# Kernel optimization log

Measured on AMD Instinct MI355X. Metric: run time of the kernel, lower is better.

## Reference

```python
import jax, jax.numpy as jnp
import numpy as np

N_NODES = 100000
N_EDGES = 800000
D_COORD = 16
N_FEAT = 8
D_IN = D_COORD * 2 + N_FEAT  # 40
H = 64
D_OUT = 16


def _mlp_params(key, sizes):
    ps = []
    for i, (a, b) in enumerate(zip(sizes[:-1], sizes[1:])):
        key, k = jax.random.split(key)
        # lecun_normal: std = 1/sqrt(fan_in)
        W = jax.random.normal(k, (a, b), dtype=jnp.float32) / jnp.sqrt(jnp.float32(a))
        ps.append(W)
        ps.append(jnp.zeros((b,), dtype=jnp.float32))
    return key, ps


def setup_inputs() -> dict:
    key = jax.random.key(0)
    k1, k2, k3, k4, key = jax.random.split(key, 5)
    coordinates = jax.random.normal(k1, (N_NODES, D_COORD), dtype=jnp.float32)
    feature_array = jax.random.normal(k2, (N_EDGES, N_FEAT), dtype=jnp.float32)
    non_fictitious = jnp.ones((N_EDGES,), dtype=jnp.float32)
    addr_from = jax.random.randint(k3, (N_EDGES,), 0, N_NODES, dtype=jnp.int32)
    addr_to = jax.random.randint(k4, (N_EDGES,), 0, N_NODES, dtype=jnp.int32)
    sizes = [D_IN, H, H, D_OUT]
    key, pf = _mlp_params(key, sizes)
    key, pt = _mlp_params(key, sizes)
    fW0, fb0, fW1, fb1, fW2, fb2 = pf
    tW0, tb0, tW1, tb1, tW2, tb2 = pt
    return dict(coordinates=coordinates, feature_array=feature_array,
                non_fictitious=non_fictitious, addr_from=addr_from, addr_to=addr_to,
                fW0=fW0, fb0=fb0, fW1=fW1, fb1=fb1, fW2=fW2, fb2=fb2,
                tW0=tW0, tb0=tb0, tW1=tW1, tb1=tb1, tW2=tW2, tb2=tb2)


def _mlp(x, W0, b0, W1, b1, W2, b2):
    # hidden activations = relu, final_activation = None
    h = jax.nn.relu(x @ W0 + b0)
    h = jax.nn.relu(h @ W1 + b1)
    return h @ W2 + b2


def reference(coordinates, feature_array, non_fictitious, addr_from, addr_to,
              fW0, fb0, fW1, fb1, fW2, fb2, tW0, tb0, tW1, tb1, tW2, tb2):
    # Shared edge input: [E, N_FEAT + 2*D_COORD] = concat(features, x_from, x_to)
    inp = jnp.concatenate(
        [feature_array, coordinates[addr_from], coordinates[addr_to]], axis=-1)
    mask = non_fictitious[:, None]  # [E, 1]
    inp = inp * mask
    acc = jnp.zeros((coordinates.shape[0], D_OUT), dtype=coordinates.dtype)
    # port 'from': its own MLP, scatter-add to addr_from
    out_f = _mlp(inp, fW0, fb0, fW1, fb1, fW2, fb2) * mask
    acc = acc.at[addr_from].add(out_f)
    # port 'to': its own MLP, scatter-add to addr_to
    out_t = _mlp(inp, tW0, tb0, tW1, tb1, tW2, tb2) * mask
    acc = acc.at[addr_to].add(out_t)
    # outer_activation = tanh
    return jnp.tanh(acc)
```

## Files before the change

### kernel.cpp

```cpp
#include <hip/hip_runtime.h>
#include <math.h>

constexpr int N_EDGES = 800000;
constexpr int D_COORD = 16;
constexpr int N_FEAT  = 8;
constexpr int D_IN    = 40;
constexpr int H       = 64;
constexpr int D_OUT   = 16;
constexpr int ET      = 64;
constexpr int XP      = 68;

__global__ __launch_bounds__(256) void edge_mlp_tiled(
    const float* __restrict__ coords,
    const float* __restrict__ feat,
    const float* __restrict__ mask,
    const int*   __restrict__ a_from,
    const int*   __restrict__ a_to,
    const float* __restrict__ fW0, const float* __restrict__ fb0,
    const float* __restrict__ fW1, const float* __restrict__ fb1,
    const float* __restrict__ fW2, const float* __restrict__ fb2,
    const float* __restrict__ tW0, const float* __restrict__ tb0,
    const float* __restrict__ tW1, const float* __restrict__ tb1,
    const float* __restrict__ tW2, const float* __restrict__ tb2,
    float* __restrict__ acc_out)
{
    __shared__ float Xs[D_IN * XP];
    __shared__ float Ws[H * H];
    __shared__ float Hs[H * XP];
    __shared__ float ms[ET];
    __shared__ int   nodes[2][ET];

    const int tid = threadIdx.x;
    const int e0  = blockIdx.x * ET;

    if (tid < ET) {
        ms[tid]       = mask[e0 + tid];
        nodes[0][tid] = a_from[e0 + tid];
        nodes[1][tid] = a_to[e0 + tid];
    }
    if (tid < 128) {
        const int e = tid >> 1, half = tid & 1;
        const float m = mask[e0 + e];
        float4 v = reinterpret_cast<const float4*>(feat)[(size_t)(e0 + e) * 2 + half];
        const int r = half * 4;
        Xs[(r + 0) * XP + e] = v.x * m;
        Xs[(r + 1) * XP + e] = v.y * m;
        Xs[(r + 2) * XP + e] = v.z * m;
        Xs[(r + 3) * XP + e] = v.w * m;
    }
    {
        const int e = tid >> 2, q = tid & 3;
        const float m = mask[e0 + e];
        const int nf = a_from[e0 + e];
        const int nt = a_to[e0 + e];
        float4 cf = reinterpret_cast<const float4*>(coords)[(size_t)nf * 4 + q];
        float4 ct = reinterpret_cast<const float4*>(coords)[(size_t)nt * 4 + q];
        const int rf = 8 + q * 4, rt = 24 + q * 4;
        Xs[(rf + 0) * XP + e] = cf.x * m;
        Xs[(rf + 1) * XP + e] = cf.y * m;
        Xs[(rf + 2) * XP + e] = cf.z * m;
        Xs[(rf + 3) * XP + e] = cf.w * m;
        Xs[(rt + 0) * XP + e] = ct.x * m;
        Xs[(rt + 1) * XP + e] = ct.y * m;
        Xs[(rt + 2) * XP + e] = ct.z * m;
        Xs[(rt + 3) * XP + e] = ct.w * m;
    }

    const int tx = tid & 15, ty = tid >> 4;

    auto run_mlp = [&](const float* __restrict__ W0, const float* __restrict__ b0,
                       const float* __restrict__ W1, const float* __restrict__ b1,
                       const float* __restrict__ W2, const float* __restrict__ b2,
                       const int which)
    {
        float a[4][4];

        __syncthreads();
        {
            const float4* s4 = reinterpret_cast<const float4*>(W0);
            float4* d4 = reinterpret_cast<float4*>(Ws);
            #pragma unroll
            for (int i = 0; i < (D_IN * H / 4 + 255) / 256; ++i) {
                int idx = tid + i * 256;
                if (idx < D_IN * H / 4) d4[idx] = s4[idx];
            }
        }
        __syncthreads();

        {
            float4 bv = reinterpret_cast<const float4*>(b0)[tx];
            #pragma unroll
            for (int i = 0; i < 4; ++i) {
                a[i][0] = bv.x; a[i][1] = bv.y; a[i][2] = bv.z; a[i][3] = bv.w;
            }
            #pragma unroll 8
            for (int k = 0; k < D_IN; ++k) {
                float4 xv = *reinterpret_cast<const float4*>(&Xs[k * XP + ty * 4]);
                float4 wv = *reinterpret_cast<const float4*>(&Ws[k * H + tx * 4]);
                const float xc[4] = {xv.x, xv.y, xv.z, xv.w};
                const float wc[4] = {wv.x, wv.y, wv.z, wv.w};
                #pragma unroll
                for (int i = 0; i < 4; ++i)
                    #pragma unroll
                    for (int j = 0; j < 4; ++j)
                        a[i][j] = fmaf(xc[i], wc[j], a[i][j]);
            }
            #pragma unroll
            for (int i = 0; i < 4; ++i)
                #pragma unroll
                for (int j = 0; j < 4; ++j)
                    a[i][j] = fmaxf(a[i][j], 0.0f);
        }
        __syncthreads();

        #pragma unroll
        for (int j = 0; j < 4; ++j) {
            const int r = tx * 4 + j;
            float4 hv = make_float4(a[0][j], a[1][j], a[2][j], a[3][j]);
            *reinterpret_cast<float4*>(&Hs[r * XP + ty * 4]) = hv;
        }
        {
            const float4* s4 = reinterpret_cast<const float4*>(W1);
            float4* d4 = reinterpret_cast<float4*>(Ws);
            #pragma unroll
            for (int i = 0; i < H * H / 4 / 256; ++i)
                d4[tid + i * 256] = s4[tid + i * 256];
        }
        __syncthreads();

        {
            float4 bv = reinterpret_cast<const float4*>(b1)[tx];
            float acc2[4][4];
            #pragma unroll
            for (int i = 0; i < 4; ++i) {
                acc2[i][0] = bv.x; acc2[i][1] = bv.y; acc2[i][2] = bv.z; acc2[i][3] = bv.w;
            }
            #pragma unroll 8
            for (int k = 0; k < H; ++k) {
                float4 xv = *reinterpret_cast<const float4*>(&Hs[k * XP + ty * 4]);
                float4 wv = *reinterpret_cast<const float4*>(&Ws[k * H + tx * 4]);
                const float xc[4] = {xv.x, xv.y, xv.z, xv.w};
                const float wc[4] = {wv.x, wv.y, wv.z, wv.w};
                #pragma unroll
                for (int i = 0; i < 4; ++i)
                    #pragma unroll
                    for (int j = 0; j < 4; ++j)
                        acc2[i][j] = fmaf(xc[i], wc[j], acc2[i][j]);
            }
            #pragma unroll
            for (int i = 0; i < 4; ++i)
                #pragma unroll
                for (int j = 0; j < 4; ++j)
                    a[i][j] = fmaxf(acc2[i][j], 0.0f);
        }
        __syncthreads();

        #pragma unroll
        for (int j = 0; j < 4; ++j) {
            const int r = tx * 4 + j;
            float4 hv = make_float4(a[0][j], a[1][j], a[2][j], a[3][j]);
            *reinterpret_cast<float4*>(&Hs[r * XP + ty * 4]) = hv;
        }
        {
            const float4* s4 = reinterpret_cast<const float4*>(W2);
            float4* d4 = reinterpret_cast<float4*>(Ws);
            if (tid < H * D_OUT / 4) d4[tid] = s4[tid];
        }
        __syncthreads();

        {
            const int ox = tid & 15, ey = tid >> 4;
            float o[4];
            const float bo = b2[ox];
            #pragma unroll
            for (int i = 0; i < 4; ++i) o[i] = bo;
            #pragma unroll 8
            for (int k = 0; k < H; ++k) {
                float4 xv = *reinterpret_cast<const float4*>(&Hs[k * XP + ey * 4]);
                const float wv = Ws[k * D_OUT + ox];
                o[0] = fmaf(xv.x, wv, o[0]);
                o[1] = fmaf(xv.y, wv, o[1]);
                o[2] = fmaf(xv.z, wv, o[2]);
                o[3] = fmaf(xv.w, wv, o[3]);
            }
            #pragma unroll
            for (int i = 0; i < 4; ++i) {
                const int e = ey * 4 + i;
                const float m = ms[e];
                const int node = nodes[which][e];
                atomicAdd(acc_out + (size_t)node * D_OUT + ox, o[i] * m);
            }
        }
    };

    run_mlp(fW0, fb0, fW1, fb1, fW2, fb2, 0);
    run_mlp(tW0, tb0, tW1, tb1, tW2, tb2, 1);
}

__global__ __launch_bounds__(256) void tanh_inplace(float* __restrict__ p, int n4)
{
    const int i = blockIdx.x * blockDim.x + threadIdx.x;
    if (i >= n4) return;
    float4 v = reinterpret_cast<float4*>(p)[i];
    v.x = tanhf(v.x); v.y = tanhf(v.y); v.z = tanhf(v.z); v.w = tanhf(v.w);
    reinterpret_cast<float4*>(p)[i] = v;
}

extern "C" void kernel_launch(void* const* d_in, const int* in_sizes, int n_in,
                              void* d_out, int out_size, void* d_ws, size_t ws_size,
                              hipStream_t stream)
{
    const float* coords = (const float*)d_in[0];
    const float* feat   = (const float*)d_in[1];
    const float* mask   = (const float*)d_in[2];
    const int*   a_from = (const int*)d_in[3];
    const int*   a_to   = (const int*)d_in[4];
    const float* fW0 = (const float*)d_in[5];
    const float* fb0 = (const float*)d_in[6];
    const float* fW1 = (const float*)d_in[7];
    const float* fb1 = (const float*)d_in[8];
    const float* fW2 = (const float*)d_in[9];
    const float* fb2 = (const float*)d_in[10];
    const float* tW0 = (const float*)d_in[11];
    const float* tb0 = (const float*)d_in[12];
    const float* tW1 = (const float*)d_in[13];
    const float* tb1 = (const float*)d_in[14];
    const float* tW2 = (const float*)d_in[15];
    const float* tb2 = (const float*)d_in[16];

    float* out = (float*)d_out;

    hipMemsetAsync(out, 0, (size_t)out_size * sizeof(float), stream);

    edge_mlp_tiled<<<N_EDGES / ET, 256, 0, stream>>>(
        coords, feat, mask, a_from, a_to,
        fW0, fb0, fW1, fb1, fW2, fb2,
        tW0, tb0, tW1, tb1, tW2, tb2, out);

    const int n4 = out_size / 4;
    tanh_inplace<<<(n4 + 255) / 256, 256, 0, stream>>>(out, n4);
}
```

Baseline: 472.9 us.

## Read MLP weights as wave-uniform scalar loads and double edges per block

Stops staging weights in shared memory. Each wavefront now owns a 16-column output slice, and its weights are read straight from global memory with wave-uniform indices, so they can become scalar loads. The edge tile grows from 64 to 128 edges per block, each lane computes 2 edges, and a launch-bounds occupancy hint is added. This removes the weight-copy stages and their barriers, at the cost of more accumulator registers per lane and reliance on the scalar cache holding the weights.

```diff
diff --git a/kernel.cpp b/kernel.cpp
--- a/kernel.cpp
+++ b/kernel.cpp
@@ -2,15 +2,12 @@
 #include <math.h>
 
 constexpr int N_EDGES = 800000;
-constexpr int D_COORD = 16;
-constexpr int N_FEAT  = 8;
 constexpr int D_IN    = 40;
 constexpr int H       = 64;
 constexpr int D_OUT   = 16;
-constexpr int ET      = 64;
-constexpr int XP      = 68;
-
-__global__ __launch_bounds__(256) void edge_mlp_tiled(
+constexpr int EB      = 128;
+
+__global__ __launch_bounds__(256, 2) void edge_mlp_v3(
     const float* __restrict__ coords,
     const float* __restrict__ feat,
     const float* __restrict__ mask,
@@ -24,171 +21,136 @@
     const float* __restrict__ tW2, const float* __restrict__ tb2,
     float* __restrict__ acc_out)
 {
-    __shared__ float Xs[D_IN * XP];
-    __shared__ float Ws[H * H];
-    __shared__ float Hs[H * XP];
-    __shared__ float ms[ET];
-    __shared__ int   nodes[2][ET];
-
-    const int tid = threadIdx.x;
-    const int e0  = blockIdx.x * ET;
-
-    if (tid < ET) {
+    __shared__ float Xs[D_IN * EB];
+    __shared__ float Hs[H * EB];
+    __shared__ float ms[EB];
+    __shared__ int   nodes[2][EB];
+
+    const int tid  = threadIdx.x;
+    const int lane = tid & 63;
+    const int uwid = __builtin_amdgcn_readfirstlane(tid >> 6);
+    const int e0   = blockIdx.x * EB;
+
+    if (tid < EB) {
         ms[tid]       = mask[e0 + tid];
         nodes[0][tid] = a_from[e0 + tid];
         nodes[1][tid] = a_to[e0 + tid];
     }
-    if (tid < 128) {
+    {
         const int e = tid >> 1, half = tid & 1;
         const float m = mask[e0 + e];
         float4 v = reinterpret_cast<const float4*>(feat)[(size_t)(e0 + e) * 2 + half];
         const int r = half * 4;
-        Xs[(r + 0) * XP + e] = v.x * m;
-        Xs[(r + 1) * XP + e] = v.y * m;
-        Xs[(r + 2) * XP + e] = v.z * m;
-        Xs[(r + 3) * XP + e] = v.w * m;
+        Xs[(r + 0) * EB + e] = v.x * m;
+        Xs[(r + 1) * EB + e] = v.y * m;
+        Xs[(r + 2) * EB + e] = v.z * m;
+        Xs[(r + 3) * EB + e] = v.w * m;
     }
     {
-        const int e = tid >> 2, q = tid & 3;
+        const int e = tid >> 1, which = tid & 1;
         const float m = mask[e0 + e];
-        const int nf = a_from[e0 + e];
-        const int nt = a_to[e0 + e];
-        float4 cf = reinterpret_cast<const float4*>(coords)[(size_t)nf * 4 + q];
-        float4 ct = reinterpret_cast<const float4*>(coords)[(size_t)nt * 4 + q];
-        const int rf = 8 + q * 4, rt = 24 + q * 4;
-        Xs[(rf + 0) * XP + e] = cf.x * m;
-        Xs[(rf + 1) * XP + e] = cf.y * m;
-        Xs[(rf + 2) * XP + e] = cf.z * m;
-        Xs[(rf + 3) * XP + e] = cf.w * m;
-        Xs[(rt + 0) * XP + e] = ct.x * m;
-        Xs[(rt + 1) * XP + e] = ct.y * m;
-        Xs[(rt + 2) * XP + e] = ct.z * m;
-        Xs[(rt + 3) * XP + e] = ct.w * m;
+        const int n = which ? a_to[e0 + e] : a_from[e0 + e];
+        const float4* c4 = reinterpret_cast<const float4*>(coords + (size_t)n * 16);
+        const int rbase = 8 + which * 16;
+        #pragma unroll
+        for (int q = 0; q < 4; ++q) {
+            float4 v = c4[q];
+            Xs[(rbase + 4*q + 0) * EB + e] = v.x * m;
+            Xs[(rbase + 4*q + 1) * EB + e] = v.y * m;
+            Xs[(rbase + 4*q + 2) * EB + e] = v.z * m;
+            Xs[(rbase + 4*q + 3) * EB + e] = v.w * m;
+        }
     }
-
-    const int tx = tid & 15, ty = tid >> 4;
+    __syncthreads();
 
     auto run_mlp = [&](const float* __restrict__ W0, const float* __restrict__ b0,
                        const float* __restrict__ W1, const float* __restrict__ b1,
                        const float* __restrict__ W2, const float* __restrict__ b2,
                        const int which)
     {
-        float a[4][4];
-
-        __syncthreads();
+        float h0[2][16];
         {
-            const float4* s4 = reinterpret_cast<const float4*>(W0);
-            float4* d4 = reinterpret_cast<float4*>(Ws);
-            #pragma unroll
-            for (int i = 0; i < (D_IN * H / 4 + 255) / 256; ++i) {
-                int idx = tid + i * 256;
-                if (idx < D_IN * H / 4) d4[idx] = s4[idx];
-            }
-        }
-        __syncthreads();
-
+            const float* __restrict__ bb = b0 + uwid * 16;
+            #pragma unroll
+            for (int j = 0; j < 16; ++j) { const float b = bb[j]; h0[0][j] = b; h0[1][j] = b; }
+            const float* __restrict__ wb = W0 + uwid * 16;
+            #pragma unroll
+            for (int k = 0; k < D_IN; ++k) {
+                const float2 xv = *reinterpret_cast<const float2*>(&Xs[k * EB + 2 * lane]);
+                const float* __restrict__ w = wb + k * H;
+                #pragma unroll
+                for (int j = 0; j < 16; ++j) {
+                    h0[0][j] = fmaf(xv.x, w[j], h0[0][j]);
+                    h0[1][j] = fmaf(xv.y, w[j], h0[1][j]);
+                }
+            }
+            #pragma unroll
+            for (int i = 0; i < 2; ++i)
+                #pragma unroll
+                for (int j = 0; j < 16; ++j) h0[i][j] = fmaxf(h0[i][j], 0.0f);
+        }
+
+        __syncthreads();
+        #pragma unroll
+        for (int j = 0; j < 16; ++j)
+            *reinterpret_cast<float2*>(&Hs[(uwid * 16 + j) * EB + 2 * lane]) =
+                make_float2(h0[0][j], h0[1][j]);
+        __syncthreads();
+
+        float h1[2][16];
         {
-            float4 bv = reinterpret_cast<const float4*>(b0)[tx];
-            #pragma unroll
-            for (int i = 0; i < 4; ++i) {
-                a[i][0] = bv.x; a[i][1] = bv.y; a[i][2] = bv.z; a[i][3] = bv.w;
-            }
-            #pragma unroll 8
-            for (int k = 0; k < D_IN; ++k) {
-                float4 xv = *reinterpret_cast<const float4*>(&Xs[k * XP + ty * 4]);
-                float4 wv = *reinterpret_cast<const float4*>(&Ws[k * H + tx * 4]);
-                const float xc[4] = {xv.x, xv.y, xv.z, xv.w};
-                const float wc[4] = {wv.x, wv.y, wv.z, wv.w};
-                #pragma unroll
-                for (int i = 0; i < 4; ++i)
-                    #pragma unroll
-                    for (int j = 0; j < 4; ++j)
-                        a[i][j] = fmaf(xc[i], wc[j], a[i][j]);
-            }
-            #pragma unroll
-            for (int i = 0; i < 4; ++i)
-                #pragma unroll
-                for (int j = 0; j < 4; ++j)
-                    a[i][j] = fmaxf(a[i][j], 0.0f);
-        }
-        __syncthreads();
-
+            const float* __restrict__ bb = b1 + uwid * 16;
+            #pragma unroll
+            for (int j = 0; j < 16; ++j) { const float b = bb[j]; h1[0][j] = b; h1[1][j] = b; }
+            const float* __restrict__ wb = W1 + uwid * 16;
+            #pragma unroll
+            for (int k = 0; k < H; ++k) {
+                const float2 xv = *reinterpret_cast<const float2*>(&Hs[k * EB + 2 * lane]);
+                const float* __restrict__ w = wb + k * H;
+                #pragma unroll
+                for (int j = 0; j < 16; ++j) {
+                    h1[0][j] = fmaf(xv.x, w[j], h1[0][j]);
+                    h1[1][j] = fmaf(xv.y, w[j], h1[1][j]);
+                }
+            }
+            #pragma unroll
+            for (int i = 0; i < 2; ++i)
+                #pragma unroll
+                for (int j = 0; j < 16; ++j) h1[i][j] = fmaxf(h1[i][j], 0.0f);
+        }
+
+        __syncthreads();
         #pragma unroll
-        for (int j = 0; j < 4; ++j) {
-            const int r = tx * 4 + j;
-            float4 hv = make_float4(a[0][j], a[1][j], a[2][j], a[3][j]);
-            *reinterpret_cast<float4*>(&Hs[r * XP + ty * 4]) = hv;
-        }
+        for (int j = 0; j < 16; ++j)
+            *reinterpret_cast<float2*>(&Hs[(uwid * 16 + j) * EB + 2 * lane]) =
+                make_float2(h1[0][j], h1[1][j]);
+        __syncthreads();
+
         {
-            const float4* s4 = reinterpret_cast<const float4*>(W1);
-            float4* d4 = reinterpret_cast<float4*>(Ws);
-            #pragma unroll
-            for (int i = 0; i < H * H / 4 / 256; ++i)
-                d4[tid + i * 256] = s4[tid + i * 256];
-        }
-        __syncthreads();
-
-        {
-            float4 bv = reinterpret_cast<const float4*>(b1)[tx];
-            float acc2[4][4];
-            #pragma unroll
-            for (int i = 0; i < 4; ++i) {
-                acc2[i][0] = bv.x; acc2[i][1] = bv.y; acc2[i][2] = bv.z; acc2[i][3] = bv.w;
-            }
-            #pragma unroll 8
+            float o[2][4];
+            const float* __restrict__ bb = b2 + uwid * 4;
+            #pragma unroll
+            for (int j = 0; j < 4; ++j) { const float b = bb[j]; o[0][j] = b; o[1][j] = b; }
+            const float* __restrict__ wb = W2 + uwid * 4;
+            #pragma unroll
             for (int k = 0; k < H; ++k) {
-                float4 xv = *reinterpret_cast<const float4*>(&Hs[k * XP + ty * 4]);
-                float4 wv = *reinterpret_cast<const float4*>(&Ws[k * H + tx * 4]);
-                const float xc[4] = {xv.x, xv.y, xv.z, xv.w};
-                const float wc[4] = {wv.x, wv.y, wv.z, wv.w};
-                #pragma unroll
-                for (int i = 0; i < 4; ++i)
-                    #pragma unroll
-                    for (int j = 0; j < 4; ++j)
-                        acc2[i][j] = fmaf(xc[i], wc[j], acc2[i][j]);
-            }
-            #pragma unroll
-            for (int i = 0; i < 4; ++i)
-                #pragma unroll
-                for (int j = 0; j < 4; ++j)
-                    a[i][j] = fmaxf(acc2[i][j], 0.0f);
-        }
-        __syncthreads();
-
-        #pragma unroll
-        for (int j = 0; j < 4; ++j) {
-            const int r = tx * 4 + j;
-            float4 hv = make_float4(a[0][j], a[1][j], a[2][j], a[3][j]);
-            *reinterpret_cast<float4*>(&Hs[r * XP + ty * 4]) = hv;
-        }
-        {
-            const float4* s4 = reinterpret_cast<const float4*>(W2);
-            float4* d4 = reinterpret_cast<float4*>(Ws);
-            if (tid < H * D_OUT / 4) d4[tid] = s4[tid];
-        }
-        __syncthreads();
-
-        {
-            const int ox = tid & 15, ey = tid >> 4;
-            float o[4];
-            const float bo = b2[ox];
-            #pragma unroll
-            for (int i = 0; i < 4; ++i) o[i] = bo;
-            #pragma unroll 8
-            for (int k = 0; k < H; ++k) {
-                float4 xv = *reinterpret_cast<const float4*>(&Hs[k * XP + ey * 4]);
-                const float wv = Ws[k * D_OUT + ox];
-                o[0] = fmaf(xv.x, wv, o[0]);
-                o[1] = fmaf(xv.y, wv, o[1]);
-                o[2] = fmaf(xv.z, wv, o[2]);
-                o[3] = fmaf(xv.w, wv, o[3]);
-            }
-            #pragma unroll
-            for (int i = 0; i < 4; ++i) {
-                const int e = ey * 4 + i;
+                const float2 xv = *reinterpret_cast<const float2*>(&Hs[k * EB + 2 * lane]);
+                const float* __restrict__ w = wb + k * D_OUT;
+                #pragma unroll
+                for (int j = 0; j < 4; ++j) {
+                    o[0][j] = fmaf(xv.x, w[j], o[0][j]);
+                    o[1][j] = fmaf(xv.y, w[j], o[1][j]);
+                }
+            }
+            #pragma unroll
+            for (int i = 0; i < 2; ++i) {
+                const int e = 2 * lane + i;
                 const float m = ms[e];
                 const int node = nodes[which][e];
-                atomicAdd(acc_out + (size_t)node * D_OUT + ox, o[i] * m);
+                float* __restrict__ dst = acc_out + (size_t)node * D_OUT + uwid * 4;
+                #pragma unroll
+                for (int j = 0; j < 4; ++j)
+                    atomicAdd(dst + j, o[i][j] * m);
             }
         }
     };
@@ -232,7 +194,7 @@
 
     hipMemsetAsync(out, 0, (size_t)out_size * sizeof(float), stream);
 
-    edge_mlp_tiled<<<N_EDGES / ET, 256, 0, stream>>>(
+    edge_mlp_v3<<<N_EDGES / EB, 256, 0, stream>>>(
         coords, feat, mask, a_from, a_to,
         fW0, fb0, fW1, fb1, fW2, fb2,
         tW0, tb0, tW1, tb1, tW2, tb2, out);
```

Result: slower. 1.479 ms (+212.7%).
